# Kernel tuning notes

Measured on AMD Instinct MI355X. Metric: run time of the kernel, lower is better.

Reference implementation:

```python
import jax, jax.numpy as jnp
import numpy as np

N_NODES = 100000
N_EDGES = 3200000
ENTITY_DIM = 128
LAYER_DIMS = [128, 64, 32]


def setup_inputs() -> dict:
    key = jax.random.key(0)
    ks = jax.random.split(key, 20)
    inp = {
        "x": jax.random.normal(ks[0], (N_NODES, ENTITY_DIM), dtype=jnp.float32) * 0.1,
        "src_idx": jax.random.randint(ks[1], (N_EDGES,), 0, N_NODES, dtype=jnp.int32),
        "dst_idx": jax.random.randint(ks[2], (N_EDGES,), 0, N_NODES, dtype=jnp.int32),
        "edge_attn": jax.random.uniform(ks[3], (N_EDGES,), dtype=jnp.float32),
    }
    in_dim = ENTITY_DIM
    ki = 4
    for li, out_dim in enumerate(LAYER_DIMS):
        scale = jnp.sqrt(2.0 / (in_dim + out_dim)).astype(jnp.float32)
        inp[f"W1_{li}"] = jax.random.normal(ks[ki], (in_dim, out_dim), dtype=jnp.float32) * scale
        inp[f"b1_{li}"] = jnp.zeros((out_dim,), dtype=jnp.float32)
        inp[f"W2_{li}"] = jax.random.normal(ks[ki + 1], (in_dim, out_dim), dtype=jnp.float32) * scale
        inp[f"b2_{li}"] = jnp.zeros((out_dim,), dtype=jnp.float32)
        ki += 2
        in_dim = out_dim
    return inp


def _kgat_layer(x, src_idx, dst_idx, a, W1, b1, W2, b2):
    # edge-weighted sparse aggregation: h_n[v] = sum_{(u->v)} a_e * x[u]
    msgs = x[src_idx] * a[:, None]                       # [E, D] gather + scale
    h_n = jax.ops.segment_sum(msgs, dst_idx, num_segments=x.shape[0])  # [N, D]
    # bi-interaction fuse
    out = jax.nn.leaky_relu((x + h_n) @ W1 + b1) + jax.nn.leaky_relu((x * h_n) @ W2 + b2)
    return out


def reference(x, src_idx, dst_idx, edge_attn,
              W1_0, b1_0, W2_0, b2_0,
              W1_1, b1_1, W2_1, b2_1,
              W1_2, b1_2, W2_2, b2_2):
    params = [(W1_0, b1_0, W2_0, b2_0), (W1_1, b1_1, W2_1, b2_1), (W1_2, b1_2, W2_2, b2_2)]
    embs = [x]
    h = x
    for (W1, b1, W2, b2) in params:
        h = _kgat_layer(h, src_idx, dst_idx, edge_attn, W1, b1, W2, b2)
        embs.append(h)
    return jnp.concatenate(embs, axis=1)  # [N, 128+128+64+32]
```

## Files before the change

### kernel.cpp

```cpp
#include <hip/hip_runtime.h>
#include <hip/hip_bf16.h>

#define LRELU_SLOPE 0.01f

typedef __attribute__((ext_vector_type(8))) short short8;
typedef __attribute__((ext_vector_type(4))) float f32x4;

__device__ __forceinline__ unsigned int f2bf_rne(float f) {
    unsigned int u = __float_as_uint(f);
    u += 0x7FFFu + ((u >> 16) & 1u);
    return u >> 16;
}
__device__ __forceinline__ float bf_lo(unsigned int u) { return __uint_as_float(u << 16); }
__device__ __forceinline__ float bf_hi(unsigned int u) { return __uint_as_float(u & 0xFFFF0000u); }

__device__ __forceinline__ unsigned int pack_edge(int src, float a) {
    int q = (int)(a * 32767.0f + 0.5f);
    q = q < 0 ? 0 : (q > 32767 ? 32767 : q);
    return ((unsigned int)src << 15) | (unsigned int)q;
}

__global__ void bucket_count_kernel(const int* __restrict__ dst,
                                    int* __restrict__ bucket_total, int E, int NB) {
    __shared__ int cnt[512];
    const int t = threadIdx.x;
    const int tile0 = blockIdx.x * 8192;
    for (int i = t; i < 512; i += 256) cnt[i] = 0;
    __syncthreads();
#pragma unroll
    for (int j = 0; j < 32; ++j) {
        int e = tile0 + j * 256 + t;
        if (e < E) atomicAdd(&cnt[dst[e] >> 8], 1);
    }
    __syncthreads();
    for (int i = t; i < NB; i += 256) {
        int c = cnt[i];
        if (c) atomicAdd(&bucket_total[i], c);
    }
}

__global__ void bucket_scan_kernel(const int* __restrict__ bucket_total,
                                   int* __restrict__ bucket_base,
                                   int* __restrict__ row_ptr, int NB, int n) {
    __shared__ int s[512];
    const int t = threadIdx.x;
    int c = (t < NB) ? bucket_total[t] : 0;
    s[t] = c;
    __syncthreads();
    for (int off = 1; off < 512; off <<= 1) {
        int v = (t >= off) ? s[t - off] : 0;
        __syncthreads();
        s[t] += v;
        __syncthreads();
    }
    if (t < NB) bucket_base[t] = s[t] - c;
    if (t == 511) {
        bucket_base[NB] = s[511];
        row_ptr[n] = s[511];
    }
}

__global__ void bucket_scatter_kernel(const int* __restrict__ dst,
                                      const int* __restrict__ src,
                                      const float* __restrict__ attn,
                                      const int* __restrict__ bucket_base,
                                      int* __restrict__ bucket_fill,
                                      int2* __restrict__ bsa,
                                      int E, int NB) {
    __shared__ int cnt[512];
    __shared__ int basef[512];
    const int t = threadIdx.x;
    const int tile0 = blockIdx.x * 4096;
    for (int i = t; i < 512; i += 256) cnt[i] = 0;
    __syncthreads();
    int d[16], lr[16];
#pragma unroll
    for (int j = 0; j < 16; ++j) {
        int e = tile0 + j * 256 + t;
        if (e < E) {
            d[j] = dst[e];
            lr[j] = atomicAdd(&cnt[d[j] >> 8], 1);
        }
    }
    __syncthreads();
    for (int i = t; i < NB; i += 256) {
        int c = cnt[i];
        int r = c ? atomicAdd(&bucket_fill[i], c) : 0;
        basef[i] = bucket_base[i] + r;
    }
    __syncthreads();
#pragma unroll
    for (int j = 0; j < 16; ++j) {
        int e = tile0 + j * 256 + t;
        if (e < E) {
            int pos = basef[d[j] >> 8] + lr[j];
            unsigned int px = ((unsigned int)src[e] << 8) | (unsigned int)(d[j] & 255);
            bsa[pos] = make_int2((int)px, __float_as_int(attn[e]));
        }
    }
}

__global__ void bucket_build_kernel(const int* __restrict__ bucket_base,
                                    const int2* __restrict__ bsa,
                                    int* __restrict__ row_ptr,
                                    unsigned int* __restrict__ csr_pk,
                                    int n, int sshift) {
    __shared__ int cnt[2048];
    __shared__ int pre[2048];
    __shared__ int cur[2048];
    __shared__ int ps[1024];
    const int t = threadIdx.x;
    const int k = blockIdx.x;
    const int base = bucket_base[k];
    const int M = bucket_base[k + 1] - base;
    const int node0 = k << 8;
    cnt[t] = 0; cnt[t + 1024] = 0;
    __syncthreads();
    for (int i = t; i < M; i += 1024) {
        int2 sa = bsa[base + i];
        unsigned int px = (unsigned int)sa.x;
        int local = (int)(px & 255u);
        int blk = (int)(px >> 8) >> sshift; blk = blk > 7 ? 7 : blk;
        atomicAdd(&cnt[(local << 3) | blk], 1);
    }
    __syncthreads();
    int a = cnt[2 * t], b = cnt[2 * t + 1];
    int pair = a + b;
    ps[t] = pair;
    __syncthreads();
    for (int off = 1; off < 1024; off <<= 1) {
        int v = (t >= off) ? ps[t - off] : 0;
        __syncthreads();
        ps[t] += v;
        __syncthreads();
    }
    int pbase = ps[t] - pair;
    pre[2 * t]     = pbase;
    pre[2 * t + 1] = pbase + a;
    cur[2 * t]     = pbase;
    cur[2 * t + 1] = pbase + a;
    __syncthreads();
    if (t < 256) {
        int dnode = node0 + t;
        if (dnode < n) row_ptr[dnode] = base + pre[t << 3];
    }
    __syncthreads();
    for (int i = t; i < M; i += 1024) {
        int2 sa = bsa[base + i];
        unsigned int px = (unsigned int)sa.x;
        int local = (int)(px & 255u);
        int srcv  = (int)(px >> 8);
        int blk = srcv >> sshift; blk = blk > 7 ? 7 : blk;
        int p = base + atomicAdd(&cur[(local << 3) | blk], 1);
        csr_pk[p] = pack_edge(srcv, __int_as_float(sa.y));
    }
}

__global__ void count_rank_kernel(const int* __restrict__ dst, int* __restrict__ counts,
                                  int* __restrict__ rank, int E) {
    const int base = blockIdx.x * (blockDim.x * 4) + threadIdx.x;
#pragma unroll
    for (int j = 0; j < 4; ++j) {
        int e = base + j * 256;
        if (e < E) rank[e] = atomicAdd(&counts[dst[e]], 1);
    }
}

__global__ void count_kernel(const int* __restrict__ dst, int* __restrict__ counts, int E) {
    int e = blockIdx.x * blockDim.x + threadIdx.x;
    if (e < E) atomicAdd(&counts[dst[e]], 1);
}

__global__ void scan_blocks_kernel(int* __restrict__ counts, int* __restrict__ row_ptr,
                                   int* __restrict__ partials, int n) {
    __shared__ int s[1024];
    const int t = threadIdx.x;
    const int i = blockIdx.x * 1024 + t;
    int c = (i < n) ? counts[i] : 0;
    s[t] = c;
    __syncthreads();
    for (int off = 1; off < 1024; off <<= 1) {
        int v = (t >= off) ? s[t - off] : 0;
        __syncthreads();
        s[t] += v;
        __syncthreads();
    }
    if (i < n) {
        row_ptr[i] = s[t] - c;
        counts[i] = 0;
    }
    if (t == 1023) partials[blockIdx.x] = s[1023];
}

__global__ void scan_partials_kernel(int* __restrict__ partials, int* __restrict__ row_ptr,
                                     int G, int n) {
    __shared__ int s[1024];
    const int t = threadIdx.x;
    int c = (t < G) ? partials[t] : 0;
    s[t] = c;
    __syncthreads();
    for (int off = 1; off < 1024; off <<= 1) {
        int v = (t >= off) ? s[t - off] : 0;
        __syncthreads();
        s[t] += v;
        __syncthreads();
    }
    if (t < G) partials[t] = s[t] - c;
    if (t == 1023) row_ptr[n] = s[1023];
}

__global__ void scan_add_kernel(int* __restrict__ row_ptr, const int* __restrict__ partials, int n) {
    int i = blockIdx.x * blockDim.x + threadIdx.x;
    if (i < n) row_ptr[i] += partials[i >> 10];
}

__global__ void fill_rank_kernel(const int* __restrict__ src, const int* __restrict__ dst,
                                 const float* __restrict__ attn,
                                 const int* __restrict__ row_ptr, const int* __restrict__ rank,
                                 unsigned int* __restrict__ csr_pk, int E) {
    const int base = blockIdx.x * (blockDim.x * 4) + threadIdx.x;
    int  e[4], d[4], r[4], s[4];
    float a[4];
    bool ok[4];
#pragma unroll
    for (int j = 0; j < 4; ++j) {
        e[j] = base + j * 256;
        ok[j] = e[j] < E;
        int idx = ok[j] ? e[j] : 0;
        d[j] = dst[idx];
        r[j] = rank[idx];
        s[j] = src[idx];
        a[j] = attn[idx];
    }
    int p[4];
#pragma unroll
    for (int j = 0; j < 4; ++j) p[j] = row_ptr[d[j]] + r[j];
#pragma unroll
    for (int j = 0; j < 4; ++j)
        if (ok[j]) csr_pk[p[j]] = pack_edge(s[j], a[j]);
}

__global__ void fill_kernel(const int* __restrict__ src, const int* __restrict__ dst,
                            const float* __restrict__ attn,
                            const int* __restrict__ row_ptr, int* __restrict__ counts,
                            int2* __restrict__ csr_edge, int E) {
    int e = blockIdx.x * blockDim.x + threadIdx.x;
    if (e < E) {
        int d = dst[e];
        int pos = row_ptr[d] + atomicAdd(&counts[d], 1);
        csr_edge[pos] = make_int2(src[e], __float_as_int(attn[e]));
    }
}

__global__ void copy_cvt_kernel(const float4* __restrict__ x, float4* __restrict__ out,
                                uint2* __restrict__ xb, int n4) {
    int i = blockIdx.x * blockDim.x + threadIdx.x;
    if (i < n4) {
        float4 v = x[i];
        int nd = i >> 5;
        int c = i & 31;
        out[(long)nd * 88 + c] = v;
        xb[i] = make_uint2(f2bf_rne(v.x) | (f2bf_rne(v.y) << 16),
                           f2bf_rne(v.z) | (f2bf_rne(v.w) << 16));
    }
}

__global__ void copy_x_kernel(const float4* __restrict__ x, float4* __restrict__ out, int n4) {
    int i = blockIdx.x * blockDim.x + threadIdx.x;
    if (i < n4) {
        int v = i >> 5;
        int c = i & 31;
        out[(long)v * 88 + c] = x[i];
    }
}

__global__ void wtrans_all_kernel(const float* __restrict__ W1_0, const float* __restrict__ W2_0,
                                  const float* __restrict__ W1_1, const float* __restrict__ W2_1,
                                  const float* __restrict__ W1_2, const float* __restrict__ W2_2,
                                  unsigned short* __restrict__ t10, unsigned short* __restrict__ t20,
                                  unsigned short* __restrict__ t11, unsigned short* __restrict__ t21,
                                  unsigned short* __restrict__ t12, unsigned short* __restrict__ t22) {
    int i = blockIdx.x * blockDim.x + threadIdx.x;
    const float* W; unsigned short* T; int in_d, out_d, base;
    if      (i < 16384) { W = W1_0; T = t10; in_d = 128; out_d = 128; base = 0; }
    else if (i < 32768) { W = W2_0; T = t20; in_d = 128; out_d = 128; base = 16384; }
    else if (i < 40960) { W = W1_1; T = t11; in_d = 128; out_d = 64;  base = 32768; }
    else if (i < 49152) { W = W2_1; T = t21; in_d = 128; out_d = 64;  base = 40960; }
    else if (i < 51200) { W = W1_2; T = t12; in_d = 64;  out_d = 32;  base = 49152; }
    else if (i < 53248) { W = W2_2; T = t22; in_d = 64;  out_d = 32;  base = 51200; }
    else return;
    int idx = i - base;
    int o = idx / in_d, k = idx - o * in_d;
    T[idx] = (unsigned short)f2bf_rne(W[(long)k * out_d + o]);
}

__global__ void agg128_bf_kernel(const unsigned int* __restrict__ xb,
                                 const int* __restrict__ row_ptr,
                                 const unsigned int* __restrict__ csr,
                                 unsigned int* __restrict__ hb, int n_nodes) {
    const int lane = threadIdx.x & 63;
    const int wid = (blockIdx.x * blockDim.x + threadIdx.x) >> 6;
    if (wid >= n_nodes) return;
    const int e0 = __builtin_amdgcn_readfirstlane(row_ptr[wid]);
    const int e1 = __builtin_amdgcn_readfirstlane(row_ptr[wid + 1]);
    float2 accA = {0.f, 0.f}, accB = {0.f, 0.f};
    int e = e0;
    for (; e + 8 <= e1; e += 8) {
        unsigned int px[8], u[8];
#pragma unroll
        for (int j = 0; j < 8; ++j) px[j] = csr[e + j];
#pragma unroll
        for (int j = 0; j < 8; ++j) u[j] = xb[(long)(px[j] >> 15) * 64 + lane];
#pragma unroll
        for (int j = 0; j < 8; ++j) {
            float q = (float)(px[j] & 32767u);
            if (j & 1) { accB.x = fmaf(q, bf_lo(u[j]), accB.x); accB.y = fmaf(q, bf_hi(u[j]), accB.y); }
            else       { accA.x = fmaf(q, bf_lo(u[j]), accA.x); accA.y = fmaf(q, bf_hi(u[j]), accA.y); }
        }
    }
    for (; e < e1; ++e) {
        unsigned int px = csr[e];
        unsigned int u = xb[(long)(px >> 15) * 64 + lane];
        float q = (float)(px & 32767u);
        accA.x = fmaf(q, bf_lo(u), accA.x); accA.y = fmaf(q, bf_hi(u), accA.y);
    }
    const float s = 1.0f / 32767.0f;
    float hx = (accA.x + accB.x) * s;
    float hy = (accA.y + accB.y) * s;
    hb[(long)wid * 64 + lane] = f2bf_rne(hx) | (f2bf_rne(hy) << 16);
}

__global__ void agg64_bf_kernel(const unsigned int* __restrict__ xb,
                                const int* __restrict__ row_ptr,
                                const unsigned int* __restrict__ csr,
                                unsigned int* __restrict__ hb, int n_nodes) {
    const int lane = threadIdx.x & 63;
    const int half = lane >> 5;
    const int l = lane & 31;
    const int wid = (blockIdx.x * blockDim.x + threadIdx.x) >> 6;
    if (wid >= n_nodes) return;
    const int e0 = __builtin_amdgcn_readfirstlane(row_ptr[wid]);
    const int e1 = __builtin_amdgcn_readfirstlane(row_ptr[wid + 1]);
    float2 accA = {0.f, 0.f}, accB = {0.f, 0.f};
    int e = e0;
    for (; e + 4 <= e1; e += 4) {
        unsigned int pA = csr[e + half];
        unsigned int pB = csr[e + 2 + half];
        unsigned int uA = xb[(long)(pA >> 15) * 32 + l];
        unsigned int uB = xb[(long)(pB >> 15) * 32 + l];
        float qA = (float)(pA & 32767u), qB = (float)(pB & 32767u);
        accA.x = fmaf(qA, bf_lo(uA), accA.x); accA.y = fmaf(qA, bf_hi(uA), accA.y);
        accB.x = fmaf(qB, bf_lo(uB), accB.x); accB.y = fmaf(qB, bf_hi(uB), accB.y);
    }
    if (e + 2 <= e1) {
        unsigned int p = csr[e + half];
        unsigned int u = xb[(long)(p >> 15) * 32 + l];
        float q = (float)(p & 32767u);
        accA.x = fmaf(q, bf_lo(u), accA.x); accA.y = fmaf(q, bf_hi(u), accA.y);
        e += 2;
    }
    if (e < e1 && half == 0) {
        unsigned int p = csr[e];
        unsigned int u = xb[(long)(p >> 15) * 32 + l];
        float q = (float)(p & 32767u);
        accA.x = fmaf(q, bf_lo(u), accA.x); accA.y = fmaf(q, bf_hi(u), accA.y);
    }
    accA.x += accB.x; accA.y += accB.y;
    accA.x += __shfl_xor(accA.x, 32);
    accA.y += __shfl_xor(accA.y, 32);
    if (half == 0) {
        const float s = 1.0f / 32767.0f;
        hb[(long)wid * 32 + l] = f2bf_rne(accA.x * s) | (f2bf_rne(accA.y * s) << 16);
    }
}

template <int D>
__global__ void agg_f32_kernel(const float* __restrict__ xin, long xstride,
                               const int* __restrict__ row_ptr,
                               const int2* __restrict__ csr_edge,
                               float* __restrict__ hagg, int n_nodes) {
    const int lane = threadIdx.x & 63;
    const int wid = (blockIdx.x * blockDim.x + threadIdx.x) >> 6;
    if (wid >= n_nodes) return;
    const int e0 = row_ptr[wid], e1 = row_ptr[wid + 1];
    if (D == 128) {
        float2 accA = {0.f, 0.f}, accB = {0.f, 0.f};
        int e = e0;
        for (; e + 2 <= e1; e += 2) {
            int2 p0 = csr_edge[e + 0];
            int2 p1 = csr_edge[e + 1];
            float2 x0 = reinterpret_cast<const float2*>(xin + (long)p0.x * xstride)[lane];
            float2 x1 = reinterpret_cast<const float2*>(xin + (long)p1.x * xstride)[lane];
            float a0 = __int_as_float(p0.y), a1 = __int_as_float(p1.y);
            accA.x = fmaf(a0, x0.x, accA.x); accA.y = fmaf(a0, x0.y, accA.y);
            accB.x = fmaf(a1, x1.x, accB.x); accB.y = fmaf(a1, x1.y, accB.y);
        }
        for (; e < e1; ++e) {
            int2 p = csr_edge[e];
            float2 xv = reinterpret_cast<const float2*>(xin + (long)p.x * xstride)[lane];
            float a = __int_as_float(p.y);
            accA.x = fmaf(a, xv.x, accA.x); accA.y = fmaf(a, xv.y, accA.y);
        }
        accA.x += accB.x; accA.y += accB.y;
        reinterpret_cast<float2*>(hagg + (long)wid * 128)[lane] = accA;
    } else {
        float accA = 0.f;
        for (int e = e0; e < e1; ++e) {
            int2 p = csr_edge[e];
            accA = fmaf(__int_as_float(p.y), xin[(long)p.x * xstride + lane], accA);
        }
        hagg[(long)wid * 64 + lane] = accA;
    }
}

template <int IN, int OUT>
__global__ __launch_bounds__(256) void mlp_mfma_kernel(
    const unsigned int* __restrict__ xin_bf,
    const unsigned int* __restrict__ hagg_bf,
    const unsigned short* __restrict__ W1T, const float* __restrict__ b1,
    const unsigned short* __restrict__ W2T, const float* __restrict__ b2,
    float* __restrict__ out, long ostride,
    unsigned short* __restrict__ xb_next, int n_nodes)
{
    constexpr int BM  = 64;
    constexpr int NCH = IN / 8;
    constexpr int KK  = IN / 32;
    constexpr int NT  = OUT / 16;
    constexpr int RU  = IN / 2;

    __shared__ uint4 xp_s[BM * NCH];
    __shared__ uint4 xm_s[BM * NCH];

    const int t = threadIdx.x;
    const int node0 = blockIdx.x * BM;

    for (int idx = t; idx < BM * NCH; idx += 256) {
        int n = idx / NCH;
        int c = idx - n * NCH;
        int v = node0 + n;
        uint4 xv = {0u,0u,0u,0u}, hv = {0u,0u,0u,0u};
        if (v < n_nodes) {
            xv = *reinterpret_cast<const uint4*>(xin_bf  + (long)v * RU + c * 4);
            hv = *reinterpret_cast<const uint4*>(hagg_bf + (long)v * RU + c * 4);
        }
        uint4 up, um;
        {
            float xl = bf_lo(xv.x), xh = bf_hi(xv.x), hl = bf_lo(hv.x), hh = bf_hi(hv.x);
            up.x = f2bf_rne(xl + hl) | (f2bf_rne(xh + hh) << 16);
            um.x = f2bf_rne(xl * hl) | (f2bf_rne(xh * hh) << 16);
        }
        {
            float xl = bf_lo(xv.y), xh = bf_hi(xv.y), hl = bf_lo(hv.y), hh = bf_hi(hv.y);
            up.y = f2bf_rne(xl + hl) | (f2bf_rne(xh + hh) << 16);
            um.y = f2bf_rne(xl * hl) | (f2bf_rne(xh * hh) << 16);
        }
        {
            float xl = bf_lo(xv.z), xh = bf_hi(xv.z), hl = bf_lo(hv.z), hh = bf_hi(hv.z);
            up.z = f2bf_rne(xl + hl) | (f2bf_rne(xh + hh) << 16);
            um.z = f2bf_rne(xl * hl) | (f2bf_rne(xh * hh) << 16);
        }
        {
            float xl = bf_lo(xv.w), xh = bf_hi(xv.w), hl = bf_lo(hv.w), hh = bf_hi(hv.w);
            up.w = f2bf_rne(xl + hl) | (f2bf_rne(xh + hh) << 16);
            um.w = f2bf_rne(xl * hl) | (f2bf_rne(xh * hh) << 16);
        }
        int sc = c ^ (n & 7);
        xp_s[n * NCH + sc] = up;
        xm_s[n * NCH + sc] = um;
    }
    __syncthreads();

    const int lane = t & 63;
    const int wv   = t >> 6;
    const int arow = lane & 15;
    const int kgrp = lane >> 4;
    const int lrow = wv * 16 + arow;

    short8 ap[KK], am[KK];
#pragma unroll
    for (int kk = 0; kk < KK; ++kk) {
        int c  = kk * 4 + kgrp;
        int sc = c ^ (lrow & 7);
        ap[kk] = *reinterpret_cast<const short8*>(&xp_s[lrow * NCH + sc]);
        am[kk] = *reinterpret_cast<const short8*>(&xm_s[lrow * NCH + sc]);
    }

    f32x4 acc1[NT], acc2[NT];
#pragma unroll
    for (int nt = 0; nt < NT; ++nt) {
        acc1[nt] = (f32x4){0.f, 0.f, 0.f, 0.f};
        acc2[nt] = (f32x4){0.f, 0.f, 0.f, 0.f};
    }

#pragma unroll
    for (int nt = 0; nt < NT; ++nt) {
        const long nb = (long)(nt * 16 + arow) * IN + kgrp * 8;
#pragma unroll
        for (int kk = 0; kk < KK; ++kk) {
            short8 bw1 = *reinterpret_cast<const short8*>(W1T + nb + kk * 32);
            acc1[nt] = __builtin_amdgcn_mfma_f32_16x16x32_bf16(ap[kk], bw1, acc1[nt], 0, 0, 0);
            short8 bw2 = *reinterpret_cast<const short8*>(W2T + nb + kk * 32);
            acc2[nt] = __builtin_amdgcn_mfma_f32_16x16x32_bf16(am[kk], bw2, acc2[nt], 0, 0, 0);
        }
    }

    const int mbase = node0 + wv * 16 + kgrp * 4;
#pragma unroll
    for (int nt = 0; nt < NT; ++nt) {
        int n = nt * 16 + arow;
        float bb1 = b1[n], bb2 = b2[n];
#pragma unroll
        for (int j = 0; j < 4; ++j) {
            int v = mbase + j;
            if (v < n_nodes) {
                float r1 = acc1[nt][j] + bb1;
                float r2 = acc2[nt][j] + bb2;
                r1 = r1 >= 0.f ? r1 : LRELU_SLOPE * r1;
                r2 = r2 >= 0.f ? r2 : LRELU_SLOPE * r2;
                float r = r1 + r2;
                out[(long)v * ostride + n] = r;
                if (xb_next) xb_next[(long)v * OUT + n] = (unsigned short)f2bf_rne(r);
            }
        }
    }
}

template <int IN, int OUT, int NT>
__global__ void mlp_kernel(const float* __restrict__ xin, long xstride,
                           const float* __restrict__ hagg,
                           const float* __restrict__ W1, const float* __restrict__ b1,
                           const float* __restrict__ W2, const float* __restrict__ b2,
                           float* __restrict__ out, long ostride,
                           unsigned short* __restrict__ xb_next, int n_nodes) {
    constexpr int SLOTS = 256 / OUT;
    constexpr int NPB = SLOTS * NT;
    __shared__ float s_xp[NPB][IN + 4];
    __shared__ float s_xm[NPB][IN + 4];
    const int t = threadIdx.x;
    const int o = t % OUT;
    const int slot = t / OUT;
    const int node0 = blockIdx.x * NPB;

    for (int idx = t; idx < NPB * (IN / 4); idx += 256) {
        int n = idx / (IN / 4), c = idx % (IN / 4);
        int k = c * 4;
        int v = node0 + n;
        float4 xv = {0.f, 0.f, 0.f, 0.f}, hv = {0.f, 0.f, 0.f, 0.f};
        if (v < n_nodes) {
            xv = *reinterpret_cast<const float4*>(xin + (long)v * xstride + k);
            hv = *reinterpret_cast<const float4*>(hagg + (long)v * IN + k);
        }
        *reinterpret_cast<float4*>(&s_xp[n][k]) =
            make_float4(xv.x + hv.x, xv.y + hv.y, xv.z + hv.z, xv.w + hv.w);
        *reinterpret_cast<float4*>(&s_xm[n][k]) =
            make_float4(xv.x * hv.x, xv.y * hv.y, xv.z * hv.z, xv.w * hv.w);
    }
    __syncthreads();

    float acc1[NT], acc2[NT];
#pragma unroll
    for (int j = 0; j < NT; ++j) { acc1[j] = 0.f; acc2[j] = 0.f; }

    for (int k = 0; k < IN; k += 4) {
        float w10 = W1[(k + 0) * OUT + o], w11 = W1[(k + 1) * OUT + o];
        float w12 = W1[(k + 2) * OUT + o], w13 = W1[(k + 3) * OUT + o];
        float w20 = W2[(k + 0) * OUT + o], w21 = W2[(k + 1) * OUT + o];
        float w22 = W2[(k + 2) * OUT + o], w23 = W2[(k + 3) * OUT + o];
#pragma unroll
        for (int j = 0; j < NT; ++j) {
            int n = slot * NT + j;
            float4 xp = *reinterpret_cast<const float4*>(&s_xp[n][k]);
            float4 xm = *reinterpret_cast<const float4*>(&s_xm[n][k]);
            acc1[j] = fmaf(xp.x, w10, acc1[j]); acc1[j] = fmaf(xp.y, w11, acc1[j]);
            acc1[j] = fmaf(xp.z, w12, acc1[j]); acc1[j] = fmaf(xp.w, w13, acc1[j]);
            acc2[j] = fmaf(xm.x, w20, acc2[j]); acc2[j] = fmaf(xm.y, w21, acc2[j]);
            acc2[j] = fmaf(xm.z, w22, acc2[j]); acc2[j] = fmaf(xm.w, w23, acc2[j]);
        }
    }

    const float bb1 = b1[o], bb2 = b2[o];
#pragma unroll
    for (int j = 0; j < NT; ++j) {
        int v = node0 + slot * NT + j;
        if (v < n_nodes) {
            float r1 = acc1[j] + bb1;
            float r2 = acc2[j] + bb2;
            r1 = r1 >= 0.f ? r1 : LRELU_SLOPE * r1;
            r2 = r2 >= 0.f ? r2 : LRELU_SLOPE * r2;
            float r = r1 + r2;
            out[(long)v * ostride + o] = r;
            if (xb_next) xb_next[(long)v * OUT + o] = (unsigned short)f2bf_rne(r);
        }
    }
}

extern "C" void kernel_launch(void* const* d_in, const int* in_sizes, int n_in,
                              void* d_out, int out_size, void* d_ws, size_t ws_size,
                              hipStream_t stream) {
    const float* x    = (const float*)d_in[0];
    const int*   src  = (const int*)d_in[1];
    const int*   dst  = (const int*)d_in[2];
    const float* attn = (const float*)d_in[3];
    const float* W1_0 = (const float*)d_in[4];
    const float* b1_0 = (const float*)d_in[5];
    const float* W2_0 = (const float*)d_in[6];
    const float* b2_0 = (const float*)d_in[7];
    const float* W1_1 = (const float*)d_in[8];
    const float* b1_1 = (const float*)d_in[9];
    const float* W2_1 = (const float*)d_in[10];
    const float* b2_1 = (const float*)d_in[11];
    const float* W1_2 = (const float*)d_in[12];
    const float* b1_2 = (const float*)d_in[13];
    const float* W2_2 = (const float*)d_in[14];
    const float* b2_2 = (const float*)d_in[15];
    float* out = (float*)d_out;

    const int N = in_sizes[0] / 128;
    const int E = in_sizes[1];

    char* w = (char*)d_ws;
    size_t off = 0;
    auto alloc = [&](size_t bytes) -> void* {
        void* p = w + off;
        off += (bytes + 511) & ~(size_t)511;
        return p;
    };
    int*          counts   = (int*)alloc((size_t)N * 4);
    int*          row_ptr  = (int*)alloc((size_t)(N + 1) * 4);
    int*          partials = (int*)alloc((size_t)1024 * 4);
    unsigned int* csr_pk   = (unsigned int*)alloc((size_t)E * 8);
    float*        h_agg    = (float*)alloc((size_t)N * 128 * 4);
    unsigned int* xb_a     = (unsigned int*)alloc((size_t)N * 128 * 2);
    unsigned int* xb_b     = (unsigned int*)alloc((size_t)N * 128 * 2);
    unsigned short* w1t0   = (unsigned short*)alloc((size_t)128 * 128 * 2);
    unsigned short* w2t0   = (unsigned short*)alloc((size_t)128 * 128 * 2);
    unsigned short* w1t1   = (unsigned short*)alloc((size_t)64 * 128 * 2);
    unsigned short* w2t1   = (unsigned short*)alloc((size_t)64 * 128 * 2);
    unsigned short* w1t2   = (unsigned short*)alloc((size_t)32 * 64 * 2);
    unsigned short* w2t2   = (unsigned short*)alloc((size_t)32 * 64 * 2);
    const bool use_bf16 = (off <= ws_size) && (N <= (1 << 17));

    const int NB = (N + 255) >> 8;
    int* bucket_mem  = (int*)alloc((size_t)2 * NB * 4);
    int* bucket_base = (int*)alloc((size_t)(NB + 1) * 4);
    const size_t off_fast = off;

    int2* bsa = (int2*)h_agg;
    const bool use_fast = use_bf16 && (off_fast <= ws_size) && (NB <= 512) &&
                          ((size_t)E * 8 <= (size_t)N * 512);

    int* rank = (int*)alloc((size_t)E * 4);
    const bool use_rank = use_bf16 && (off <= ws_size);

    const int G = (N + 1023) / 1024;
    unsigned int* h_bf = (unsigned int*)h_agg;

    int sshift = 0;
    while (((N - 1) >> sshift) > 7) ++sshift;

    if (use_fast) {
        int* bucket_total = bucket_mem;
        int* bucket_fill  = bucket_mem + NB;
        hipMemsetAsync(bucket_mem, 0, (size_t)2 * NB * 4, stream);
        bucket_count_kernel<<<(E + 8191) / 8192, 256, 0, stream>>>(dst, bucket_total, E, NB);
        bucket_scan_kernel<<<1, 512, 0, stream>>>(bucket_total, bucket_base, row_ptr, NB, N);
        bucket_scatter_kernel<<<(E + 4095) / 4096, 256, 0, stream>>>(
            dst, src, attn, bucket_base, bucket_fill, bsa, E, NB);
        bucket_build_kernel<<<NB, 1024, 0, stream>>>(bucket_base, bsa, row_ptr, csr_pk, N, sshift);
    } else if (use_bf16) {
        hipMemsetAsync(counts, 0, (size_t)N * 4, stream);
        count_rank_kernel<<<(E + 1023) / 1024, 256, 0, stream>>>(dst, counts, rank, E);
        scan_blocks_kernel<<<G, 1024, 0, stream>>>(counts, row_ptr, partials, N);
        scan_partials_kernel<<<1, 1024, 0, stream>>>(partials, row_ptr, G, N);
        scan_add_kernel<<<(N + 255) / 256, 256, 0, stream>>>(row_ptr, partials, N);
        fill_rank_kernel<<<(E + 1023) / 1024, 256, 0, stream>>>(src, dst, attn, row_ptr,
                                                                rank, csr_pk, E);
    } else {
        hipMemsetAsync(counts, 0, (size_t)N * 4, stream);
        count_kernel<<<(E + 255) / 256, 256, 0, stream>>>(dst, counts, E);
        scan_blocks_kernel<<<G, 1024, 0, stream>>>(counts, row_ptr, partials, N);
        scan_partials_kernel<<<1, 1024, 0, stream>>>(partials, row_ptr, G, N);
        scan_add_kernel<<<(N + 255) / 256, 256, 0, stream>>>(row_ptr, partials, N);
        fill_kernel<<<(E + 255) / 256, 256, 0, stream>>>(src, dst, attn, row_ptr, counts,
                                                         (int2*)csr_pk, E);
    }

    if (use_bf16) {
        copy_cvt_kernel<<<(N * 32 + 255) / 256, 256, 0, stream>>>(
            (const float4*)x, (float4*)out, (uint2*)xb_a, N * 32);
        wtrans_all_kernel<<<208, 256, 0, stream>>>(W1_0, W2_0, W1_1, W2_1, W1_2, W2_2,
                                                   w1t0, w2t0, w1t1, w2t1, w1t2, w2t2);

        agg128_bf_kernel<<<(N + 3) / 4, 256, 0, stream>>>(xb_a, row_ptr, csr_pk, h_bf, N);
        mlp_mfma_kernel<128, 128><<<(N + 63) / 64, 256, 0, stream>>>(
            xb_a, h_bf, w1t0, b1_0, w2t0, b2_0,
            out + 128, 352, (unsigned short*)xb_b, N);
        agg128_bf_kernel<<<(N + 3) / 4, 256, 0, stream>>>(xb_b, row_ptr, csr_pk, h_bf, N);
        mlp_mfma_kernel<128, 64><<<(N + 63) / 64, 256, 0, stream>>>(
            xb_b, h_bf, w1t1, b1_1, w2t1, b2_1,
            out + 256, 352, (unsigned short*)xb_a, N);
        agg64_bf_kernel<<<(N + 3) / 4, 256, 0, stream>>>(xb_a, row_ptr, csr_pk, h_bf, N);
        mlp_mfma_kernel<64, 32><<<(N + 63) / 64, 256, 0, stream>>>(
            xb_a, h_bf, w1t2, b1_2, w2t2, b2_2,
            out + 320, 352, (unsigned short*)nullptr, N);
    } else {
        copy_x_kernel<<<(N * 32 + 255) / 256, 256, 0, stream>>>((const float4*)x, (float4*)out, N * 32);
        agg_f32_kernel<128><<<(N + 3) / 4, 256, 0, stream>>>(x, 128, row_ptr, (const int2*)csr_pk, h_agg, N);
        mlp_kernel<128, 128, 4><<<(N + 7) / 8, 256, 0, stream>>>(x, 128, h_agg,
                                                                 W1_0, b1_0, W2_0, b2_0,
                                                                 out + 128, 352,
                                                                 (unsigned short*)nullptr, N);
        agg_f32_kernel<128><<<(N + 3) / 4, 256, 0, stream>>>(out + 128, 352, row_ptr, (const int2*)csr_pk, h_agg, N);
        mlp_kernel<128, 64, 4><<<(N + 15) / 16, 256, 0, stream>>>(out + 128, 352, h_agg,
                                                                  W1_1, b1_1, W2_1, b2_1,
                                                                  out + 256, 352,
                                                                  (unsigned short*)nullptr, N);
        agg_f32_kernel<64><<<(N + 3) / 4, 256, 0, stream>>>(out + 256, 352, row_ptr, (const int2*)csr_pk, h_agg, N);
        mlp_kernel<64, 32, 4><<<(N + 31) / 32, 256, 0, stream>>>(out + 256, 352, h_agg,
                                                                 W1_2, b1_2, W2_2, b2_2,
                                                                 out + 320, 352,
                                                                 (unsigned short*)nullptr, N);
    }
}
```

Baseline: 806.3 us.

## Aggregate by source-block phases using per-block row pointers in bucketed CSR

The bucket build now orders edges as (source block, local destination) and writes a full per-bucket 2048-entry row-pointer table. New aggregation kernels have each wave own 16 destination nodes and sweep the 8 source blocks in order. All concurrent waves in a phase then read from the same slice of the feature table, which should improve L2 locality of the gathers. The costs are 16 register accumulators per lane, serial per-node loops with little unrolling, and a larger row-pointer array. The agg64 fallback path is also simplified.

```diff
diff --git a/kernel.cpp b/kernel.cpp
--- a/kernel.cpp
+++ b/kernel.cpp
@@ -41,7 +41,7 @@
 
 __global__ void bucket_scan_kernel(const int* __restrict__ bucket_total,
                                    int* __restrict__ bucket_base,
-                                   int* __restrict__ row_ptr, int NB, int n) {
+                                   int* __restrict__ rp2, int NB) {
     __shared__ int s[512];
     const int t = threadIdx.x;
     int c = (t < NB) ? bucket_total[t] : 0;
@@ -56,7 +56,7 @@
     if (t < NB) bucket_base[t] = s[t] - c;
     if (t == 511) {
         bucket_base[NB] = s[511];
-        row_ptr[n] = s[511];
+        rp2[(long)NB * 2048] = s[511];
     }
 }
 
@@ -102,9 +102,9 @@
 
 __global__ void bucket_build_kernel(const int* __restrict__ bucket_base,
                                     const int2* __restrict__ bsa,
-                                    int* __restrict__ row_ptr,
+                                    int* __restrict__ rp2,
                                     unsigned int* __restrict__ csr_pk,
-                                    int n, int sshift) {
+                                    int sshift) {
     __shared__ int cnt[2048];
     __shared__ int pre[2048];
     __shared__ int cur[2048];
@@ -113,7 +113,6 @@
     const int k = blockIdx.x;
     const int base = bucket_base[k];
     const int M = bucket_base[k + 1] - base;
-    const int node0 = k << 8;
     cnt[t] = 0; cnt[t + 1024] = 0;
     __syncthreads();
     for (int i = t; i < M; i += 1024) {
@@ -121,7 +120,7 @@
         unsigned int px = (unsigned int)sa.x;
         int local = (int)(px & 255u);
         int blk = (int)(px >> 8) >> sshift; blk = blk > 7 ? 7 : blk;
-        atomicAdd(&cnt[(local << 3) | blk], 1);
+        atomicAdd(&cnt[(blk << 8) | local], 1);
     }
     __syncthreads();
     int a = cnt[2 * t], b = cnt[2 * t + 1];
@@ -140,19 +139,117 @@
     cur[2 * t]     = pbase;
     cur[2 * t + 1] = pbase + a;
     __syncthreads();
-    if (t < 256) {
-        int dnode = node0 + t;
-        if (dnode < n) row_ptr[dnode] = base + pre[t << 3];
-    }
-    __syncthreads();
+    rp2[(long)k * 2048 + t]        = base + pre[t];
+    rp2[(long)k * 2048 + t + 1024] = base + pre[t + 1024];
     for (int i = t; i < M; i += 1024) {
         int2 sa = bsa[base + i];
         unsigned int px = (unsigned int)sa.x;
         int local = (int)(px & 255u);
         int srcv  = (int)(px >> 8);
         int blk = srcv >> sshift; blk = blk > 7 ? 7 : blk;
-        int p = base + atomicAdd(&cur[(local << 3) | blk], 1);
+        int p = base + atomicAdd(&cur[(blk << 8) | local], 1);
         csr_pk[p] = pack_edge(srcv, __int_as_float(sa.y));
+    }
+}
+
+__global__ __launch_bounds__(256, 8) void agg128_bkt_kernel(
+    const unsigned int* __restrict__ xb,
+    const int* __restrict__ rp2,
+    const unsigned int* __restrict__ csr,
+    unsigned int* __restrict__ hb, int n_nodes)
+{
+    const int lane = threadIdx.x & 63;
+    const int wv = threadIdx.x >> 6;
+    const int k = blockIdx.x >> 2;
+    const int qtr = blockIdx.x & 3;
+    const int dloc0 = qtr * 64 + wv * 16;
+    const int dbase = (k << 8) + dloc0;
+    const int* rpb = rp2 + (long)k * 2048;
+
+    float2 acc[16];
+#pragma unroll
+    for (int s = 0; s < 16; ++s) acc[s] = make_float2(0.f, 0.f);
+
+    for (int blk = 0; blk < 8; ++blk) {
+        const int kb = (blk << 8) | dloc0;
+#pragma unroll
+        for (int s = 0; s < 16; ++s) {
+            int e0 = __builtin_amdgcn_readfirstlane(rpb[kb + s]);
+            int e1 = __builtin_amdgcn_readfirstlane(rpb[kb + s + 1]);
+            int e = e0;
+            for (; e + 2 <= e1; e += 2) {
+                unsigned int p0 = csr[e], p1 = csr[e + 1];
+                unsigned int u0 = xb[(long)(p0 >> 15) * 64 + lane];
+                unsigned int u1 = xb[(long)(p1 >> 15) * 64 + lane];
+                float q0 = (float)(p0 & 32767u), q1 = (float)(p1 & 32767u);
+                acc[s].x = fmaf(q0, bf_lo(u0), acc[s].x);
+                acc[s].y = fmaf(q0, bf_hi(u0), acc[s].y);
+                acc[s].x = fmaf(q1, bf_lo(u1), acc[s].x);
+                acc[s].y = fmaf(q1, bf_hi(u1), acc[s].y);
+            }
+            if (e < e1) {
+                unsigned int p = csr[e];
+                unsigned int u = xb[(long)(p >> 15) * 64 + lane];
+                float q = (float)(p & 32767u);
+                acc[s].x = fmaf(q, bf_lo(u), acc[s].x);
+                acc[s].y = fmaf(q, bf_hi(u), acc[s].y);
+            }
+        }
+    }
+    const float sc = 1.0f / 32767.0f;
+#pragma unroll
+    for (int s = 0; s < 16; ++s) {
+        int d = dbase + s;
+        if (d < n_nodes)
+            hb[(long)d * 64 + lane] =
+                f2bf_rne(acc[s].x * sc) | (f2bf_rne(acc[s].y * sc) << 16);
+    }
+}
+
+__global__ __launch_bounds__(256, 8) void agg64_bkt_kernel(
+    const unsigned int* __restrict__ xb,
+    const int* __restrict__ rp2,
+    const unsigned int* __restrict__ csr,
+    unsigned int* __restrict__ hb, int n_nodes)
+{
+    const int lane = threadIdx.x & 63;
+    const int l = lane & 31;
+    const int half = lane >> 5;
+    const int wv = threadIdx.x >> 6;
+    const int k = blockIdx.x >> 2;
+    const int qtr = blockIdx.x & 3;
+    const int dloc0 = qtr * 64 + wv * 16;
+    const int dbase = (k << 8) + dloc0;
+    const int* rpb = rp2 + (long)k * 2048;
+
+    float2 acc[16];
+#pragma unroll
+    for (int s = 0; s < 16; ++s) acc[s] = make_float2(0.f, 0.f);
+
+    for (int blk = 0; blk < 8; ++blk) {
+        const int kb = (blk << 8) | dloc0;
+#pragma unroll
+        for (int s = 0; s < 16; ++s) {
+            int e0 = __builtin_amdgcn_readfirstlane(rpb[kb + s]);
+            int e1 = __builtin_amdgcn_readfirstlane(rpb[kb + s + 1]);
+            for (int e = e0 + half; e < e1; e += 2) {
+                unsigned int p = csr[e];
+                unsigned int u = xb[(long)(p >> 15) * 32 + l];
+                float q = (float)(p & 32767u);
+                acc[s].x = fmaf(q, bf_lo(u), acc[s].x);
+                acc[s].y = fmaf(q, bf_hi(u), acc[s].y);
+            }
+        }
+    }
+    const float sc = 1.0f / 32767.0f;
+#pragma unroll
+    for (int s = 0; s < 16; ++s) {
+        acc[s].x += __shfl_xor(acc[s].x, 32);
+        acc[s].y += __shfl_xor(acc[s].y, 32);
+        int d = dbase + s;
+        if (half == 0 && d < n_nodes)
+            hb[(long)d * 32 + l] =
+                f2bf_rne(acc[s].x * sc) | (f2bf_rne(acc[s].y * sc) << 16);
     }
 }
 
@@ -341,31 +438,13 @@
     if (wid >= n_nodes) return;
     const int e0 = __builtin_amdgcn_readfirstlane(row_ptr[wid]);
     const int e1 = __builtin_amdgcn_readfirstlane(row_ptr[wid + 1]);
-    float2 accA = {0.f, 0.f}, accB = {0.f, 0.f};
-    int e = e0;
-    for (; e + 4 <= e1; e += 4) {
-        unsigned int pA = csr[e + half];
-        unsigned int pB = csr[e + 2 + half];
-        unsigned int uA = xb[(long)(pA >> 15) * 32 + l];
-        unsigned int uB = xb[(long)(pB >> 15) * 32 + l];
-        float qA = (float)(pA & 32767u), qB = (float)(pB & 32767u);
-        accA.x = fmaf(qA, bf_lo(uA), accA.x); accA.y = fmaf(qA, bf_hi(uA), accA.y);
-        accB.x = fmaf(qB, bf_lo(uB), accB.x); accB.y = fmaf(qB, bf_hi(uB), accB.y);
-    }
-    if (e + 2 <= e1) {
-        unsigned int p = csr[e + half];
-        unsigned int u = xb[(long)(p >> 15) * 32 + l];
-        float q = (float)(p & 32767u);
-        accA.x = fmaf(q, bf_lo(u), accA.x); accA.y = fmaf(q, bf_hi(u), accA.y);
-        e += 2;
-    }
-    if (e < e1 && half == 0) {
+    float2 accA = {0.f, 0.f};
+    for (int e = e0 + half; e < e1; e += 2) {
         unsigned int p = csr[e];
         unsigned int u = xb[(long)(p >> 15) * 32 + l];
         float q = (float)(p & 32767u);
         accA.x = fmaf(q, bf_lo(u), accA.x); accA.y = fmaf(q, bf_hi(u), accA.y);
     }
-    accA.x += accB.x; accA.y += accB.y;
     accA.x += __shfl_xor(accA.x, 32);
     accA.y += __shfl_xor(accA.y, 32);
     if (half == 0) {
@@ -643,6 +722,7 @@
     const int NB = (N + 255) >> 8;
     int* bucket_mem  = (int*)alloc((size_t)2 * NB * 4);
     int* bucket_base = (int*)alloc((size_t)(NB + 1) * 4);
+    int* rp2         = (int*)alloc(((size_t)NB * 2048 + 1) * 4);
     const size_t off_fast = off;
 
     int2* bsa = (int2*)h_agg;
@@ -651,6 +731,7 @@
 
     int* rank = (int*)alloc((size_t)E * 4);
     const bool use_rank = use_bf16 && (off <= ws_size);
+    (void)use_rank;
 
     const int G = (N + 1023) / 1024;
     unsigned int* h_bf = (unsigned int*)h_agg;
@@ -663,10 +744,10 @@
         int* bucket_fill  = bucket_mem + NB;
         hipMemsetAsync(bucket_mem, 0, (size_t)2 * NB * 4, stream);
         bucket_count_kernel<<<(E + 8191) / 8192, 256, 0, stream>>>(dst, bucket_total, E, NB);
-        bucket_scan_kernel<<<1, 512, 0, stream>>>(bucket_total, bucket_base, row_ptr, NB, N);
+        bucket_scan_kernel<<<1, 512, 0, stream>>>(bucket_total, bucket_base, rp2, NB);
         bucket_scatter_kernel<<<(E + 4095) / 4096, 256, 0, stream>>>(
             dst, src, attn, bucket_base, bucket_fill, bsa, E, NB);
-        bucket_build_kernel<<<NB, 1024, 0, stream>>>(bucket_base, bsa, row_ptr, csr_pk, N, sshift);
+        bucket_build_kernel<<<NB, 1024, 0, stream>>>(bucket_base, bsa, rp2, csr_pk, sshift);
     } else if (use_bf16) {
         hipMemsetAsync(counts, 0, (size_t)N * 4, stream);
         count_rank_kernel<<<(E + 1023) / 1024, 256, 0, stream>>>(dst, counts, rank, E);
@@ -691,18 +772,33 @@
         wtrans_all_kernel<<<208, 256, 0, stream>>>(W1_0, W2_0, W1_1, W2_1, W1_2, W2_2,
                                                    w1t0, w2t0, w1t1, w2t1, w1t2, w2t2);
 
-        agg128_bf_kernel<<<(N + 3) / 4, 256, 0, stream>>>(xb_a, row_ptr, csr_pk, h_bf, N);
-        mlp_mfma_kernel<128, 128><<<(N + 63) / 64, 256, 0, stream>>>(
-            xb_a, h_bf, w1t0, b1_0, w2t0, b2_0,
-            out + 128, 352, (unsigned short*)xb_b, N);
-        agg128_bf_kernel<<<(N + 3) / 4, 256, 0, stream>>>(xb_b, row_ptr, csr_pk, h_bf, N);
-        mlp_mfma_kernel<128, 64><<<(N + 63) / 64, 256, 0, stream>>>(
-            xb_b, h_bf, w1t1, b1_1, w2t1, b2_1,
-            out + 256, 352, (unsigned short*)xb_a, N);
-        agg64_bf_kernel<<<(N + 3) / 4, 256, 0, stream>>>(xb_a, row_ptr, csr_pk, h_bf, N);
-        mlp_mfma_kernel<64, 32><<<(N + 63) / 64, 256, 0, stream>>>(
-            xb_a, h_bf, w1t2, b1_2, w2t2, b2_2,
-            out + 320, 352, (unsigned short*)nullptr, N);
+        if (use_fast) {
+            agg128_bkt_kernel<<<NB * 4, 256, 0, stream>>>(xb_a, rp2, csr_pk, h_bf, N);
+            mlp_mfma_kernel<128, 128><<<(N + 63) / 64, 256, 0, stream>>>(
+                xb_a, h_bf, w1t0, b1_0, w2t0, b2_0,
+                out + 128, 352, (unsigned short*)xb_b, N);
+            agg128_bkt_kernel<<<NB * 4, 256, 0, stream>>>(xb_b, rp2, csr_pk, h_bf, N);
+            mlp_mfma_kernel<128, 64><<<(N + 63) / 64, 256, 0, stream>>>(
+                xb_b, h_bf, w1t1, b1_1, w2t1, b2_1,
+                out + 256, 352, (unsigned short*)xb_a, N);
+            agg64_bkt_kernel<<<NB * 4, 256, 0, stream>>>(xb_a, rp2, csr_pk, h_bf, N);
+            mlp_mfma_kernel<64, 32><<<(N + 63) / 64, 256, 0, stream>>>(
+                xb_a, h_bf, w1t2, b1_2, w2t2, b2_2,
+                out + 320, 352, (unsigned short*)nullptr, N);
+        } else {
+            agg128_bf_kernel<<<(N + 3) / 4, 256, 0, stream>>>(xb_a, row_ptr, csr_pk, h_bf, N);
+            mlp_mfma_kernel<128, 128><<<(N + 63) / 64, 256, 0, stream>>>(
+                xb_a, h_bf, w1t0, b1_0, w2t0, b2_0,
+                out + 128, 352, (unsigned short*)xb_b, N);
+            agg128_bf_kernel<<<(N + 3) / 4, 256, 0, stream>>>(xb_b, row_ptr, csr_pk, h_bf, N);
+            mlp_mfma_kernel<128, 64><<<(N + 63) / 64, 256, 0, stream>>>(
+                xb_b, h_bf, w1t1, b1_1, w2t1, b2_1,
+                out + 256, 352, (unsigned short*)xb_a, N);
+            agg64_bf_kernel<<<(N + 3) / 4, 256, 0, stream>>>(xb_a, row_ptr, csr_pk, h_bf, N);
+            mlp_mfma_kernel<64, 32><<<(N + 63) / 64, 256, 0, stream>>>(
+                xb_a, h_bf, w1t2, b1_2, w2t2, b2_2,
+                out + 320, 352, (unsigned short*)nullptr, N);
+        }
     } else {
         copy_x_kernel<<<(N * 32 + 255) / 256, 256, 0, stream>>>((const float4*)x, (float4*)out, N * 32);
         agg_f32_kernel<128><<<(N + 3) / 4, 256, 0, stream>>>(x, 128, row_ptr, (const int2*)csr_pk, h_agg, N);
```

Result: slower. 998.3 us (+23.8%).
